# Performance work log

Hardware: AMD Instinct MI355X
Metric: run time of the kernel (lower is better)

## Reference

```python
import jax, jax.numpy as jnp
import numpy as np

BITS = 4
PACK = 32 // BITS            # 8 nibbles per int32
IN, OUT = 4096, 4096
NNZ = 75008


def setup_inputs() -> dict:
    key = jax.random.key(0)
    ks = jax.random.split(key, 7)
    x = jax.random.normal(ks[0], (4, 2048, IN), jnp.float32)
    # packed 4-bit indices: any int32 bit pattern is valid after masking
    qweight = jax.random.randint(ks[1], (IN // PACK, OUT), 0, 2147483647, jnp.int32)
    lookup_table = jax.random.normal(ks[2], (OUT, 2 ** BITS), jnp.float32)
    bias = jax.random.normal(ks[3], (OUT,), jnp.float32)
    rows = jnp.sort(jax.random.randint(ks[4], (OUT + 1,), 0, NNZ, jnp.int32))
    outlier_rows = rows.at[0].set(0).at[-1].set(NNZ)  # valid CSR crow
    outlier_cols = jax.random.randint(ks[5], (NNZ,), 0, IN, jnp.int32)
    outlier_vals = jax.random.normal(ks[6], (NNZ,), jnp.float32)
    return {
        'x': x,
        'lookup_table': lookup_table,
        'bias': bias,
        'outlier_vals': outlier_vals,
        'qweight': qweight,
        'outlier_rows': outlier_rows,
        'outlier_cols': outlier_cols,
    }


def _dequant_weight(qweight, lookup_table):
    # unpack 8 4-bit indices per int32 along the packed-infeatures axis
    shifts = (jnp.arange(PACK, dtype=jnp.int32) * BITS)
    idx = ((qweight[:, None, :] >> shifts[None, :, None]) & 0xF)  # [IN//8, 8, OUT]
    idx = idx.reshape(IN, OUT)                                     # [IN, OUT]
    # per-output-channel LUT gather: W[o, i] = lut[o, idx[i, o]]
    return jnp.take_along_axis(lookup_table, idx.T, axis=1)       # [OUT, IN]


def reference(x, lookup_table, bias, outlier_vals, qweight, outlier_rows, outlier_cols):
    W = _dequant_weight(qweight, lookup_table)
    # CSR outlier correction: scatter-add sparse values into the dense weight
    row_ids = jnp.clip(
        jnp.searchsorted(outlier_rows, jnp.arange(NNZ, dtype=jnp.int32), side='right') - 1,
        0, OUT - 1)
    W = W.at[row_ids, outlier_cols].add(outlier_vals)
    x2 = x.reshape(-1, IN)
    y = x2 @ W.T + bias                                            # [B, OUT]
    return y.reshape(x.shape[:-1] + (OUT,))
```

## Files before the change

kernel.cpp:

```cpp
#include <hip/hip_runtime.h>
#include <stdint.h>

#define IN_F  4096
#define OUT_F 4096

typedef unsigned short u16;
typedef __attribute__((ext_vector_type(8))) short bf16x8;
typedef __attribute__((ext_vector_type(4))) float f32x4;

__device__ __forceinline__ u16 f2bf(float f) {
    union { float f; unsigned u; } c; c.f = f;
    unsigned u = c.u;
    return (u16)((u + 0x7FFFu + ((u >> 16) & 1u)) >> 16);
}
__device__ __forceinline__ float bf2f(u16 h) {
    union { unsigned u; float f; } c; c.u = ((unsigned)h) << 16;
    return c.f;
}

__device__ __forceinline__ void load_lds16(const void* g, void* l) {
    unsigned loff = (unsigned)(uintptr_t)l;
    loff = (unsigned)__builtin_amdgcn_readfirstlane((int)loff);
    __builtin_amdgcn_global_load_lds(
        (const __attribute__((address_space(1))) void*)(uintptr_t)g,
        (__attribute__((address_space(3))) void*)(uintptr_t)loff,
        16, 0, 0);
}

#define DQ_O 64
#define DQ_I 256

__global__ __launch_bounds__(256) void dequant_k(const int* __restrict__ qw,
                                                 const float* __restrict__ lut,
                                                 const int* __restrict__ rows,
                                                 const int* __restrict__ cols,
                                                 const float* __restrict__ vals,
                                                 u16* __restrict__ W) {
    __shared__ __align__(16) u16 sW[DQ_O * DQ_I];
    __shared__ u16 slut[DQ_O * 18];

    const int tid = threadIdx.x;
    const int o0 = blockIdx.y * DQ_O;
    const int i0 = blockIdx.x * DQ_I;
    const int p0 = i0 >> 3;

    {
        const int idx = tid * 4;
        const float4 v = *(const float4*)(lut + (size_t)o0 * 16 + idx);
        u16* d = slut + (idx >> 4) * 18 + (idx & 15);
        d[0] = f2bf(v.x); d[1] = f2bf(v.y); d[2] = f2bf(v.z); d[3] = f2bf(v.w);
    }
    __syncthreads();

    const int o_l = tid & 63;
    const int swz = o_l & 31;
#pragma unroll
    for (int it = 0; it < 8; ++it) {
        const int p = (tid >> 6) + it * 4;
        const unsigned w = (unsigned)qw[(size_t)(p0 + p) * OUT_F + (o0 + o_l)];
        union { u16 h[8]; uint4 v; } u;
#pragma unroll
        for (int j = 0; j < 8; ++j)
            u.h[j] = slut[o_l * 18 + ((w >> (4 * j)) & 15u)];
        *(uint4*)(sW + o_l * DQ_I + ((p ^ swz) << 3)) = u.v;
    }
    __syncthreads();

    if (tid < DQ_O) {
        const int s = rows[o0 + tid], e = rows[o0 + tid + 1];
        for (int k = s; k < e; ++k) {
            const unsigned j = (unsigned)(cols[k] - i0);
            if (j < DQ_I) {
                u16* p16 = sW + tid * DQ_I + (((j >> 3) ^ swz) << 3) + (j & 7);
                *p16 = f2bf(bf2f(*p16) + vals[k]);
            }
        }
    }
    __syncthreads();

    const int ch = tid & 31;
#pragma unroll
    for (int it = 0; it < 8; ++it) {
        const int r = (tid >> 5) + it * 8;
        *(uint4*)(W + (size_t)(o0 + r) * IN_F + i0 + ch * 8) =
            *(const uint4*)(sW + r * DQ_I + ((ch ^ (r & 31)) << 3));
    }
}

__global__ __launch_bounds__(256) void cvtx_k(const float4* __restrict__ x,
                                              u16* __restrict__ xb) {
    const size_t i = (size_t)blockIdx.x * 256 + threadIdx.x;
    const float4 a = x[2 * i];
    const float4 b = x[2 * i + 1];
    union { u16 h[8]; uint4 v; } u;
    u.h[0] = f2bf(a.x); u.h[1] = f2bf(a.y); u.h[2] = f2bf(a.z); u.h[3] = f2bf(a.w);
    u.h[4] = f2bf(b.x); u.h[5] = f2bf(b.y); u.h[6] = f2bf(b.z); u.h[7] = f2bf(b.w);
    *(uint4*)(xb + i * 8) = u.v;
}

#define BM 128
#define BN 128
#define BK 32
#define GK 4096

__global__ __launch_bounds__(256) void gemm_k(const u16* __restrict__ A,
                                              const u16* __restrict__ B,
                                              const float* __restrict__ bias,
                                              float* __restrict__ C,
                                              int M, int N) {
    __shared__ __align__(16) u16 sA[BM * BK];
    __shared__ __align__(16) u16 sB[BN * BK];

    const int tid  = threadIdx.x;
    const int wave = tid >> 6;
    const int lane = tid & 63;
    const int bm = blockIdx.y * BM;
    const int bn = blockIdx.x * BN;

    const int srow = wave * 16 + (lane >> 2);
    const int scol = (lane & 3) * 8;

    const u16* ga0 = A + (size_t)(bm + srow) * GK + scol;
    const u16* ga1 = ga0 + (size_t)64 * GK;
    const u16* gb0 = B + (size_t)(bn + srow) * GK + scol;
    const u16* gb1 = gb0 + (size_t)64 * GK;

    u16* la0 = sA + wave * 512;
    u16* la1 = la0 + 2048;
    u16* lb0 = sB + wave * 512;
    u16* lb1 = lb0 + 2048;

    const int frow = lane & 15;
    const int fk   = (lane >> 4) * 8;

    const int wm = (wave >> 1) * 64;
    const int wn = (wave & 1) * 64;

    f32x4 acc[4][4] = {};

    for (int k0 = 0; k0 < GK; k0 += BK) {
        __syncthreads();
        load_lds16(ga0 + k0, la0);
        load_lds16(ga1 + k0, la1);
        load_lds16(gb0 + k0, lb0);
        load_lds16(gb1 + k0, lb1);
        __syncthreads();

        bf16x8 af[4], bfr[4];
#pragma unroll
        for (int t = 0; t < 4; ++t) {
            af[t]  = *(const bf16x8*)(sA + (wm + t * 16 + frow) * BK + fk);
            bfr[t] = *(const bf16x8*)(sB + (wn + t * 16 + frow) * BK + fk);
        }
#pragma unroll
        for (int i = 0; i < 4; ++i)
#pragma unroll
            for (int j = 0; j < 4; ++j)
                acc[i][j] = __builtin_amdgcn_mfma_f32_16x16x32_bf16(
                    af[i], bfr[j], acc[i][j], 0, 0, 0);
    }

    const int cm = bm + wm;
    const int cn = bn + wn;
#pragma unroll
    for (int j = 0; j < 4; ++j) {
        const int col = cn + j * 16 + (lane & 15);
        const float bv = bias[col];
#pragma unroll
        for (int i = 0; i < 4; ++i) {
            const int r0 = cm + i * 16 + (lane >> 4) * 4;
#pragma unroll
            for (int r = 0; r < 4; ++r)
                C[(size_t)(r0 + r) * N + col] = acc[i][j][r] + bv;
        }
    }
}

extern "C" void kernel_launch(void* const* d_in, const int* in_sizes, int n_in,
                              void* d_out, int out_size, void* d_ws, size_t ws_size,
                              hipStream_t stream) {
    (void)n_in; (void)out_size; (void)ws_size;
    const float* x     = (const float*)d_in[0];
    const float* lut   = (const float*)d_in[1];
    const float* bias  = (const float*)d_in[2];
    const float* ovals = (const float*)d_in[3];
    const int*   qw    = (const int*)d_in[4];
    const int*   orows = (const int*)d_in[5];
    const int*   ocols = (const int*)d_in[6];
    float* y = (float*)d_out;

    const int M = in_sizes[0] / IN_F;

    u16* W  = (u16*)d_ws;
    u16* xb = (u16*)((char*)d_ws + (size_t)OUT_F * IN_F * 2);

    dim3 dq_grid(IN_F / DQ_I, OUT_F / DQ_O);
    dequant_k<<<dq_grid, 256, 0, stream>>>(qw, lut, orows, ocols, ovals, W);
    cvtx_k<<<(size_t)M * IN_F / 8 / 256, 256, 0, stream>>>((const float4*)x, xb);
    dim3 grid(OUT_F / BN, M / BM);
    gemm_k<<<grid, 256, 0, stream>>>(xb, W, bias, y, M, OUT_F);
}
```

Measured before the change: 560.5 us.

## Replace GEMM with 256x256 tile, 4-stage LDS pipeline, 8-wave split-phase MFMA kernel

Replaces the simple 128x128 single-buffered GEMM with a 512-thread kernel computing 256x256 tiles with BK=32. It keeps a 4-slot ring of direct-to-LDS loads, uses XOR-swizzled LDS rows, sets MFMA priority, and uses an XCD-aware block remap. The intent is to overlap global loads with compute, raise arithmetic intensity per tile, and cut LDS bank conflicts. In exchange it adds heavy register pressure (32 accumulators), 128KB of LDS and hand-tuned waitcnt/barrier choreography that may be fragile.

```diff
diff --git a/kernel.cpp b/kernel.cpp
--- a/kernel.cpp
+++ b/kernel.cpp
@@ -98,80 +98,146 @@
     *(uint4*)(xb + i * 8) = u.v;
 }
 
-#define BM 128
-#define BN 128
-#define BK 32
 #define GK 4096
 
-__global__ __launch_bounds__(256) void gemm_k(const u16* __restrict__ A,
-                                              const u16* __restrict__ B,
-                                              const float* __restrict__ bias,
-                                              float* __restrict__ C,
-                                              int M, int N) {
-    __shared__ __align__(16) u16 sA[BM * BK];
-    __shared__ __align__(16) u16 sB[BN * BK];
+#define MF(A_, B_, C_) __builtin_amdgcn_mfma_f32_16x16x32_bf16(A_, B_, C_, 0, 0, 0)
+
+#define ROW(M_, AV)                                   \
+    acc[M_][0] = MF(AV, b0, acc[M_][0]);              \
+    acc[M_][1] = MF(AV, b1, acc[M_][1]);              \
+    acc[M_][2] = MF(AV, b2, acc[M_][2]);              \
+    acc[M_][3] = MF(AV, b3, acc[M_][3]);
+
+#define STAGE_A(SLOT, KC) do {                                              \
+    load_lds16(srcA0 + (KC) * 64, ldsA + (SLOT) * 16384 + ldst);            \
+    load_lds16(srcA1 + (KC) * 64, ldsA + (SLOT) * 16384 + 8192 + ldst);     \
+  } while (0)
+#define STAGE_B(SLOT, KC) do {                                              \
+    load_lds16(srcB0 + (KC) * 64, ldsB + (SLOT) * 16384 + ldst);            \
+    load_lds16(srcB1 + (KC) * 64, ldsB + (SLOT) * 16384 + 8192 + ldst);     \
+  } while (0)
+
+#define WAIT4 asm volatile("s_waitcnt vmcnt(4)" ::: "memory")
+#define VNOP  ((void)0)
+
+#define PH_LO(SLOT, STAGE, WAIT)                                            \
+  { const char* pa = ldsA + (SLOT) * 16384;                                 \
+    const char* pb = ldsB + (SLOT) * 16384;                                 \
+    a0 = *(const bf16x8*)(pa + offA0);                                      \
+    a1 = *(const bf16x8*)(pa + offA1);                                      \
+    a2 = *(const bf16x8*)(pa + offA2);                                      \
+    a3 = *(const bf16x8*)(pa + offA3);                                      \
+    b0 = *(const bf16x8*)(pb + offB0);                                      \
+    b1 = *(const bf16x8*)(pb + offB1);                                      \
+    b2 = *(const bf16x8*)(pb + offB2);                                      \
+    b3 = *(const bf16x8*)(pb + offB3);                                      \
+    STAGE;                                                                  \
+    __builtin_amdgcn_s_barrier();                                           \
+    asm volatile("s_waitcnt lgkmcnt(0)" ::: "memory");                      \
+    __builtin_amdgcn_s_setprio(1);                                          \
+    ROW(0, a0) ROW(1, a1) ROW(2, a2) ROW(3, a3)                             \
+    __builtin_amdgcn_s_setprio(0);                                          \
+    WAIT;                                                                   \
+    __builtin_amdgcn_s_barrier(); }
+
+#define PH_HI(SLOT, STAGE, WAIT)                                            \
+  { const char* pa = ldsA + (SLOT) * 16384;                                 \
+    a0 = *(const bf16x8*)(pa + offA4);                                      \
+    a1 = *(const bf16x8*)(pa + offA5);                                      \
+    a2 = *(const bf16x8*)(pa + offA6);                                      \
+    a3 = *(const bf16x8*)(pa + offA7);                                      \
+    STAGE;                                                                  \
+    __builtin_amdgcn_s_barrier();                                           \
+    asm volatile("s_waitcnt lgkmcnt(0)" ::: "memory");                      \
+    __builtin_amdgcn_s_setprio(1);                                          \
+    ROW(4, a0) ROW(5, a1) ROW(6, a2) ROW(7, a3)                             \
+    __builtin_amdgcn_s_setprio(0);                                          \
+    WAIT;                                                                   \
+    __builtin_amdgcn_s_barrier(); }
+
+__global__ __launch_bounds__(512, 2) void gemm8_k(const u16* __restrict__ A,
+                                                  const u16* __restrict__ B,
+                                                  const float* __restrict__ bias,
+                                                  float* __restrict__ C,
+                                                  int M, int N) {
+    __shared__ __align__(16) u16 sAq[4 * 256 * 32];
+    __shared__ __align__(16) u16 sBq[4 * 256 * 32];
 
     const int tid  = threadIdx.x;
     const int wave = tid >> 6;
     const int lane = tid & 63;
-    const int bm = blockIdx.y * BM;
-    const int bn = blockIdx.x * BN;
-
-    const int srow = wave * 16 + (lane >> 2);
-    const int scol = (lane & 3) * 8;
-
-    const u16* ga0 = A + (size_t)(bm + srow) * GK + scol;
-    const u16* ga1 = ga0 + (size_t)64 * GK;
-    const u16* gb0 = B + (size_t)(bn + srow) * GK + scol;
-    const u16* gb1 = gb0 + (size_t)64 * GK;
-
-    u16* la0 = sA + wave * 512;
-    u16* la1 = la0 + 2048;
-    u16* lb0 = sB + wave * 512;
-    u16* lb1 = lb0 + 2048;
+
+    const int ntx = N >> 8;
+    const int nwg = (M >> 8) * ntx;
+    const int cpx = nwg >> 3;
+    const int bid = blockIdx.x;
+    const int wg  = (bid & 7) * cpx + (bid >> 3);
+    const int bm = (wg / ntx) << 8;
+    const int bn = (wg % ntx) << 8;
+
+    const int r4  = tid >> 2;
+    const int cbs = ((tid & 3) << 4) ^ (((r4 >> 1) & 3) << 4);
+    const char* srcA0 = (const char*)A + ((size_t)(bm + r4) * GK) * 2 + cbs;
+    const char* srcA1 = (const char*)A + ((size_t)(bm + 128 + r4) * GK) * 2 + cbs;
+    const char* srcB0 = (const char*)B + ((size_t)(bn + r4) * GK) * 2 + cbs;
+    const char* srcB1 = (const char*)B + ((size_t)(bn + 128 + r4) * GK) * 2 + cbs;
+
+    char* ldsA = (char*)sAq;
+    char* ldsB = (char*)sBq;
+    const int ldst = wave << 10;
 
     const int frow = lane & 15;
-    const int fk   = (lane >> 4) * 8;
-
-    const int wm = (wave >> 1) * 64;
-    const int wn = (wave & 1) * 64;
-
-    f32x4 acc[4][4] = {};
-
-    for (int k0 = 0; k0 < GK; k0 += BK) {
-        __syncthreads();
-        load_lds16(ga0 + k0, la0);
-        load_lds16(ga1 + k0, la1);
-        load_lds16(gb0 + k0, lb0);
-        load_lds16(gb1 + k0, lb1);
-        __syncthreads();
-
-        bf16x8 af[4], bfr[4];
-#pragma unroll
-        for (int t = 0; t < 4; ++t) {
-            af[t]  = *(const bf16x8*)(sA + (wm + t * 16 + frow) * BK + fk);
-            bfr[t] = *(const bf16x8*)(sB + (wn + t * 16 + frow) * BK + fk);
-        }
-#pragma unroll
-        for (int i = 0; i < 4; ++i)
-#pragma unroll
-            for (int j = 0; j < 4; ++j)
-                acc[i][j] = __builtin_amdgcn_mfma_f32_16x16x32_bf16(
-                    af[i], bfr[j], acc[i][j], 0, 0, 0);
-    }
-
-    const int cm = bm + wm;
-    const int cn = bn + wn;
-#pragma unroll
-    for (int j = 0; j < 4; ++j) {
-        const int col = cn + j * 16 + (lane & 15);
+    const int fk2  = (lane >> 4) << 4;
+    const int wmr  = (wave >> 2) << 7;
+    const int wnr  = (wave & 3) << 6;
+#define AOFF(m_) ((((wmr + (m_) * 16 + frow)) << 6) + \
+                  (fk2 ^ ((((wmr + (m_) * 16 + frow) >> 1) & 3) << 4)))
+#define BOFF(n_) ((((wnr + (n_) * 16 + frow)) << 6) + \
+                  (fk2 ^ ((((wnr + (n_) * 16 + frow) >> 1) & 3) << 4)))
+    const int offA0 = AOFF(0), offA1 = AOFF(1), offA2 = AOFF(2), offA3 = AOFF(3);
+    const int offA4 = AOFF(4), offA5 = AOFF(5), offA6 = AOFF(6), offA7 = AOFF(7);
+    const int offB0 = BOFF(0), offB1 = BOFF(1), offB2 = BOFF(2), offB3 = BOFF(3);
+#undef AOFF
+#undef BOFF
+
+    f32x4 acc[8][4] = {};
+    bf16x8 a0, a1, a2, a3, b0, b1, b2, b3;
+
+    STAGE_A(0, 0); STAGE_B(0, 0);
+    STAGE_A(1, 1); STAGE_B(1, 1);
+    STAGE_A(2, 2); STAGE_B(2, 2);
+    WAIT4;
+    __builtin_amdgcn_s_barrier();
+
+    for (int it = 0; it < 32; ++it) {
+        const int c   = it * 4;
+        const int kc3 = c + 3;
+        const int kc4 = (c + 4) & 127;
+        const int kc5 = (c + 5) & 127;
+        const int kc6 = (c + 6) & 127;
+
+        PH_LO(0, STAGE_A(3, kc3), VNOP)
+        PH_HI(0, STAGE_B(3, kc3), VNOP)
+        PH_LO(1, STAGE_A(0, kc4), VNOP)
+        PH_HI(1, STAGE_B(0, kc4), WAIT4)
+        PH_LO(2, STAGE_A(1, kc5), VNOP)
+        PH_HI(2, STAGE_B(1, kc5), VNOP)
+        PH_LO(3, STAGE_A(2, kc6), VNOP)
+        PH_HI(3, STAGE_B(2, kc6), WAIT4)
+    }
+
+    const int cm = bm + wmr;
+    const int cn = bn + wnr;
+#pragma unroll
+    for (int n = 0; n < 4; ++n) {
+        const int col = cn + n * 16 + frow;
         const float bv = bias[col];
 #pragma unroll
-        for (int i = 0; i < 4; ++i) {
-            const int r0 = cm + i * 16 + (lane >> 4) * 4;
+        for (int m = 0; m < 8; ++m) {
+            const int r0 = cm + m * 16 + (lane >> 4) * 4;
 #pragma unroll
             for (int r = 0; r < 4; ++r)
-                C[(size_t)(r0 + r) * N + col] = acc[i][j][r] + bv;
+                C[(size_t)(r0 + r) * N + col] = acc[m][n][r] + bv;
         }
     }
 }
@@ -197,6 +263,7 @@
     dim3 dq_grid(IN_F / DQ_I, OUT_F / DQ_O);
     dequant_k<<<dq_grid, 256, 0, stream>>>(qw, lut, orows, ocols, ovals, W);
     cvtx_k<<<(size_t)M * IN_F / 8 / 256, 256, 0, stream>>>((const float4*)x, xb);
-    dim3 grid(OUT_F / BN, M / BM);
-    gemm_k<<<grid, 256, 0, stream>>>(xb, W, bias, y, M, OUT_F);
-}
+
+    const int nwg = (M / 256) * (OUT_F / 256);
+    gemm8_k<<<dim3(nwg), dim3(512), 0, stream>>>(xb, W, bias, y, M, OUT_F);
+}
```

New measurement: 497.8 us. 11.2% less time.
